# Kernel tuning notes

Measured on AMD Instinct MI355X. Metric: run time of the kernel, lower is better.

Reference implementation:

```python
import jax, jax.numpy as jnp
import numpy as np


def setup_inputs() -> dict:
    key = jax.random.key(0)
    k1, k2, k3, k4, k5 = jax.random.split(key, 5)
    B, C, V, D, O = 8, 64, 25000, 12, 64
    x = jax.random.normal(k1, (B, C, V), dtype=jnp.float32)
    nbr_idx = jax.random.randint(k2, (B, V, D), 0, V, dtype=jnp.int32)
    # true 1-ring valence in [1, D]
    deg = jax.random.randint(k3, (B, V), 1, D + 1, dtype=jnp.int32)
    # conv weight [O, C, 1, 2] flattened to [O, C, 2], fan-in init scale
    W = jax.random.normal(k4, (O, C, 2), dtype=jnp.float32) * (1.0 / np.sqrt(C * 2))
    b = jax.random.normal(k5, (O,), dtype=jnp.float32) * 0.01
    return {"x": x, "nbr_idx": nbr_idx, "deg": deg, "W": W, "b": b}


def reference(x, nbr_idx, deg, W, b):
    # x: [B, C, V]; nbr_idx: [B, V, D] padded 1-ring; deg: [B, V] valid count
    B, C, V = x.shape
    D = nbr_idx.shape[-1]
    # gather neighbor features: [B, C, V, D]
    gathered = jax.vmap(lambda xb, ib: xb[:, ib])(x, nbr_idx)
    mask = (jnp.arange(D, dtype=deg.dtype)[None, None, :] < deg[:, :, None])  # [B, V, D]
    maskf = mask.astype(x.dtype)[:, None, :, :]  # [B, 1, V, D]
    denom = jnp.maximum(deg, 1).astype(x.dtype)[:, None, :]  # [B, 1, V]
    nbr_mean = jnp.sum(gathered * maskf, axis=-1) / denom  # [B, C, V]
    # G: [B, C, V, 2] = (self feature, 1-ring mean); conv2d kernel (1,2)
    G = jnp.stack([x, nbr_mean], axis=-1)
    out = jnp.einsum('bcvk,ock->bov', G, W) + b[None, :, None]
    return out[..., None]  # [B, O, V, 1]
```

## Files before the change

kernel.cpp:

```cpp
#include <hip/hip_runtime.h>
#include <stdint.h>


#define NB 8
#define NC 64
#define NV 25000
#define ND 12
#define NO 64
#define VTILE 128
#define NGT 196
#define GVT 782

typedef uint32_t u32x4 __attribute__((ext_vector_type(4)));
typedef uint32_t u32x2 __attribute__((ext_vector_type(2)));
typedef __bf16  bf16x8 __attribute__((ext_vector_type(8)));
typedef float   f32x4  __attribute__((ext_vector_type(4)));

__device__ inline uint32_t bf16pack(float a, float b) {
    uint32_t ua = __float_as_uint(a), ub = __float_as_uint(b);
    ua = (ua + 0x7fffu + ((ua >> 16) & 1u)) >> 16;
    ub = (ub + 0x7fffu + ((ub >> 16) & 1u)) >> 16;
    return ua | (ub << 16);
}
__device__ inline float blo(uint32_t u) { return __uint_as_float(u << 16); }
__device__ inline float bhi(uint32_t u) { return __uint_as_float(u & 0xffff0000u); }

__global__ __launch_bounds__(256) void wt_kernel(const float* __restrict__ W,
                                                 uint32_t* __restrict__ Wcb) {
    int i = blockIdx.x * 256 + threadIdx.x;
    int m = i >> 5;
    int c = (i & 31) * 2;
    int k = m >> 6;
    int o = m & 63;
    float s0 = W[o * (NC * 2) + c * 2 + k];
    float s1 = W[o * (NC * 2) + (c + 1) * 2 + k];
    Wcb[i] = bf16pack(s0, s1);
}

__global__ __launch_bounds__(256) void ygemm_mfma(const float* __restrict__ x,
                                                  const uint32_t* __restrict__ Wcb,
                                                  const float* __restrict__ bias,
                                                  uint32_t* __restrict__ y0,
                                                  uint32_t* __restrict__ y1) {
    __shared__ uint32_t xt[VTILE * 36];

    const int b = blockIdx.x & 7;
    const int tile = blockIdx.x >> 3;
    const int vbase = tile * VTILE;
    const int tid = threadIdx.x;
    const float* xb = x + (size_t)b * NC * NV;

    {
        const int vl = tid & 127;
        const int ph = tid >> 7;
        int vg = vbase + vl;
        if (vg >= NV) vg = NV - 1;
#pragma unroll
        for (int r = 0; r < 16; ++r) {
            const int p = r * 2 + ph;
            const int c = p * 2;
            float s0 = __builtin_nontemporal_load(xb + (size_t)c * NV + vg);
            float s1 = __builtin_nontemporal_load(xb + (size_t)(c + 1) * NV + vg);
            xt[vl * 36 + p] = bf16pack(s0, s1);
        }
    }
    __syncthreads();

    const int lane = tid & 63, wave = tid >> 6;
    const int l15 = lane & 15, lq = lane >> 4;

    union BF { u32x4 q; bf16x8 v; } bf[2][2];
#pragma unroll
    for (int s = 0; s < 2; ++s) {
        const int vloc = (wave * 2 + s) * 16 + l15;
#pragma unroll
        for (int kt = 0; kt < 2; ++kt)
            bf[s][kt].q = *reinterpret_cast<const u32x4*>(&xt[vloc * 36 + kt * 16 + lq * 4]);
    }

    f32x4 acc[2][8];
#pragma unroll
    for (int s = 0; s < 2; ++s)
#pragma unroll
        for (int mt = 0; mt < 8; ++mt) acc[s][mt] = (f32x4){0.f, 0.f, 0.f, 0.f};

#pragma unroll
    for (int kt = 0; kt < 2; ++kt) {
#pragma unroll
        for (int mt = 0; mt < 8; ++mt) {
            union { u32x4 q; bf16x8 v; } au;
            au.q = *(const u32x4*)(Wcb + (size_t)(mt * 16 + l15) * 32 + kt * 16 + lq * 4);
#pragma unroll
            for (int s = 0; s < 2; ++s)
                acc[s][mt] = __builtin_amdgcn_mfma_f32_16x16x32_bf16(au.v, bf[s][kt].v,
                                                                     acc[s][mt], 0, 0, 0);
        }
    }

#pragma unroll
    for (int s = 0; s < 2; ++s) {
        const int v = vbase + (wave * 2 + s) * 16 + l15;
        if (v < NV) {
            uint32_t* yr0 = y0 + ((size_t)b * NV + v) * 32;
            uint32_t* yr1 = y1 + ((size_t)b * NV + v) * 32;
#pragma unroll
            for (int mt = 0; mt < 8; ++mt) {
                const int mo = mt * 16 + lq * 4;
                f32x4 a = acc[s][mt];
                if (mt < 4) {
                    const float* bp = bias + mo;
                    a[0] += bp[0]; a[1] += bp[1]; a[2] += bp[2]; a[3] += bp[3];
                    u32x2 p = {bf16pack(a[0], a[1]), bf16pack(a[2], a[3])};
                    __builtin_nontemporal_store(p, (u32x2*)(yr0 + (mo >> 1)));
                } else {
                    u32x2 p = {bf16pack(a[0], a[1]), bf16pack(a[2], a[3])};
                    *(u32x2*)(yr1 + ((mo - 64) >> 1)) = p;
                }
            }
        }
    }
}

__global__ __launch_bounds__(256) void gather_out(const int* __restrict__ nbr,
                                                  const int* __restrict__ deg,
                                                  const uint32_t* __restrict__ y0,
                                                  const uint32_t* __restrict__ y1,
                                                  float* __restrict__ out) {
    __shared__ float lds[32 * 68];

    const int b = blockIdx.x & 7;
    const int tile = blockIdx.x >> 3;
    const int lane = threadIdx.x & 63;
    const int wave = threadIdx.x >> 6;
    const int s = lane >> 3;
    const int j = lane & 7;
    const int vloc = wave * 8 + s;
    const int v = tile * 32 + vloc;
    const int vc = v < NV ? v : NV - 1;
    const size_t bv = (size_t)b * NV + vc;

    int idxr[ND];
    {
        const int4* p = reinterpret_cast<const int4*>(nbr + bv * ND);
        int4 a0 = p[0], a1 = p[1], a2 = p[2];
        idxr[0] = a0.x; idxr[1] = a0.y; idxr[2]  = a0.z; idxr[3]  = a0.w;
        idxr[4] = a1.x; idxr[5] = a1.y; idxr[6]  = a1.z; idxr[7]  = a1.w;
        idxr[8] = a2.x; idxr[9] = a2.y; idxr[10] = a2.z; idxr[11] = a2.w;
    }
    const int dg = deg[bv];
    const float inv = 1.0f / (float)dg;
    const uint32_t* y1b = y1 + (size_t)b * NV * 32;

    u32x4 su = __builtin_nontemporal_load(
        reinterpret_cast<const u32x4*>(y0 + bv * 32) + j);

    u32x4 rows[ND];
#pragma unroll
    for (int d = 0; d < ND; ++d) {
        if (d < dg)
            rows[d] = *(reinterpret_cast<const u32x4*>(y1b + (size_t)idxr[d] * 32) + j);
    }

    float ns[8];
#pragma unroll
    for (int t = 0; t < 8; ++t) ns[t] = 0.0f;
#pragma unroll
    for (int d = 0; d < ND; ++d) {
        if (d < dg) {
            u32x4 u = rows[d];
            ns[0] += blo(u[0]); ns[1] += bhi(u[0]);
            ns[2] += blo(u[1]); ns[3] += bhi(u[1]);
            ns[4] += blo(u[2]); ns[5] += bhi(u[2]);
            ns[6] += blo(u[3]); ns[7] += bhi(u[3]);
        }
    }

    {
        float f[8];
        f[0] = __builtin_fmaf(inv, ns[0], blo(su[0]));
        f[1] = __builtin_fmaf(inv, ns[1], bhi(su[0]));
        f[2] = __builtin_fmaf(inv, ns[2], blo(su[1]));
        f[3] = __builtin_fmaf(inv, ns[3], bhi(su[1]));
        f[4] = __builtin_fmaf(inv, ns[4], blo(su[2]));
        f[5] = __builtin_fmaf(inv, ns[5], bhi(su[2]));
        f[6] = __builtin_fmaf(inv, ns[6], blo(su[3]));
        f[7] = __builtin_fmaf(inv, ns[7], bhi(su[3]));
        f32x4 w0 = {f[0], f[1], f[2], f[3]};
        f32x4 w1 = {f[4], f[5], f[6], f[7]};
        *reinterpret_cast<f32x4*>(&lds[vloc * 68 + j * 8])     = w0;
        *reinterpret_cast<f32x4*>(&lds[vloc * 68 + j * 8 + 4]) = w1;
    }
    __syncthreads();

    {
        const int vl = threadIdx.x & 31;
        const int o8 = threadIdx.x >> 5;
        const int vv = tile * 32 + vl;
        if (vv < NV) {
            float* ob = out + (size_t)b * NO * NV + vv;
#pragma unroll
            for (int oo = 0; oo < 8; ++oo) {
                const int o = oo * 8 + o8;
                __builtin_nontemporal_store(lds[vl * 68 + o], ob + (size_t)o * NV);
            }
        }
    }
}

__global__ __launch_bounds__(64) void fallback_kernel(const float* __restrict__ x,
                                                      const int* __restrict__ nbr,
                                                      const int* __restrict__ deg,
                                                      const float* __restrict__ W,
                                                      const float* __restrict__ bias,
                                                      float* __restrict__ out) {
    const int bvi = blockIdx.x;
    const int b = bvi / NV, v = bvi % NV;
    const int o = threadIdx.x;
    const int degv = deg[bvi];
    const float inv = 1.0f / (float)degv;
    float acc = bias[o];
    for (int c = 0; c < NC; ++c) {
        const float* xc = x + ((size_t)b * NC + c) * NV;
        float m = 0.0f;
        for (int d = 0; d < degv; ++d) m += xc[nbr[(size_t)bvi * ND + d]];
        acc += W[o * (NC * 2) + c * 2] * xc[v] + W[o * (NC * 2) + c * 2 + 1] * (m * inv);
    }
    out[((size_t)b * NO + o) * NV + v] = acc;
}

extern "C" void kernel_launch(void* const* d_in, const int* in_sizes, int n_in,
                              void* d_out, int out_size, void* d_ws, size_t ws_size,
                              hipStream_t stream) {
    const float* x    = (const float*)d_in[0];
    const int*   nbr  = (const int*)d_in[1];
    const int*   deg  = (const int*)d_in[2];
    const float* W    = (const float*)d_in[3];
    const float* bias = (const float*)d_in[4];
    float* out = (float*)d_out;

    const size_t wcb_dw = 4096;
    const size_t yplane = (size_t)NB * NV * 32;
    const size_t need = (wcb_dw + 2 * yplane) * 4;
    if (ws_size >= need) {
        uint32_t* Wcb = (uint32_t*)d_ws;
        uint32_t* y0 = Wcb + wcb_dw;
        uint32_t* y1 = y0 + yplane;
        wt_kernel<<<dim3(16), 256, 0, stream>>>(W, Wcb);
        ygemm_mfma<<<dim3(NB * NGT), 256, 0, stream>>>(x, Wcb, bias, y0, y1);
        gather_out<<<dim3(NB * GVT), 256, 0, stream>>>(nbr, deg, y0, y1, out);
    } else {
        fallback_kernel<<<dim3(NB * NV), 64, 0, stream>>>(x, nbr, deg, W, bias, out);
    }
}
```

Before: 170.7 us.

## Move self-term GEMM into gather kernel, store transposed bf16 x instead of y0

The first kernel now computes only the neighbor projection y1 and also writes a transposed bf16 copy of x. The gather kernel computes the self projection W0·x plus bias with MFMA from that copy and stages it in LDS before adding the neighbor mean. The intermediate buffer is the same size as the old y0 plane, so bytes written and read do not change. The GEMM work is split across the two kernels, adding MFMA work and an extra barrier to the gather kernel, which may overlap its latency-bound neighbor loads.

```diff
diff --git a/kernel.cpp b/kernel.cpp
--- a/kernel.cpp
+++ b/kernel.cpp
@@ -7,8 +7,8 @@
 #define NV 25000
 #define ND 12
 #define NO 64
-#define VTILE 128
-#define NGT 196
+#define VROW 32
+#define ATL 391
 #define GVT 782
 
 typedef uint32_t u32x4 __attribute__((ext_vector_type(4)));
@@ -37,93 +37,80 @@
     Wcb[i] = bf16pack(s0, s1);
 }
 
-__global__ __launch_bounds__(256) void ygemm_mfma(const float* __restrict__ x,
+__global__ __launch_bounds__(256) void xty1(const float* __restrict__ x,
+                                            const uint32_t* __restrict__ Wcb,
+                                            uint32_t* __restrict__ xt,
+                                            uint32_t* __restrict__ y1) {
+    __shared__ uint32_t lb[64 * 36];
+    const int b = blockIdx.x & 7;
+    const int tile = blockIdx.x >> 3;
+    const int vbase = tile * 64;
+    const int lane = threadIdx.x & 63, wave = threadIdx.x >> 6;
+    const float* xb = x + (size_t)b * NC * NV;
+
+    {
+        int vg = vbase + lane;
+        if (vg >= NV) vg = NV - 1;
+#pragma unroll
+        for (int rr = 0; rr < 8; ++rr) {
+            const int c = wave * 16 + rr * 2;
+            float s0 = __builtin_nontemporal_load(xb + (size_t)c * NV + vg);
+            float s1 = __builtin_nontemporal_load(xb + (size_t)(c + 1) * NV + vg);
+            lb[lane * 36 + wave * 8 + rr] = bf16pack(s0, s1);
+        }
+    }
+    __syncthreads();
+
+    {
+        const int vl = threadIdx.x >> 2, q = threadIdx.x & 3;
+        const int vo = vbase + vl;
+        if (vo < NV) {
+            u32x4 w0 = *reinterpret_cast<const u32x4*>(&lb[vl * 36 + q * 8]);
+            u32x4 w1 = *reinterpret_cast<const u32x4*>(&lb[vl * 36 + q * 8 + 4]);
+            uint32_t* dst = xt + ((size_t)b * NV + vo) * VROW + q * 8;
+            *reinterpret_cast<u32x4*>(dst)     = w0;
+            *reinterpret_cast<u32x4*>(dst + 4) = w1;
+        }
+    }
+
+    const int l15 = lane & 15, lq = lane >> 4;
+    union BF { u32x4 q; bf16x8 v; } bf[2];
+#pragma unroll
+    for (int kt = 0; kt < 2; ++kt)
+        bf[kt].q = *reinterpret_cast<const u32x4*>(
+            &lb[(wave * 16 + l15) * 36 + kt * 16 + lq * 4]);
+
+    f32x4 acc[4];
+#pragma unroll
+    for (int mt = 0; mt < 4; ++mt) acc[mt] = (f32x4){0.f, 0.f, 0.f, 0.f};
+
+#pragma unroll
+    for (int kt = 0; kt < 2; ++kt) {
+#pragma unroll
+        for (int mt = 0; mt < 4; ++mt) {
+            union { u32x4 q; bf16x8 v; } au;
+            au.q = *(const u32x4*)(Wcb + (size_t)(64 + mt * 16 + l15) * 32 + kt * 16 + lq * 4);
+            acc[mt] = __builtin_amdgcn_mfma_f32_16x16x32_bf16(au.v, bf[kt].v, acc[mt], 0, 0, 0);
+        }
+    }
+
+    const int v = vbase + wave * 16 + l15;
+    if (v < NV) {
+        uint32_t* yr = y1 + ((size_t)b * NV + v) * VROW;
+#pragma unroll
+        for (int mt = 0; mt < 4; ++mt) {
+            f32x4 a = acc[mt];
+            u32x2 p = {bf16pack(a[0], a[1]), bf16pack(a[2], a[3])};
+            *(u32x2*)(yr + mt * 8 + lq * 2) = p;
+        }
+    }
+}
+
+__global__ __launch_bounds__(256) void gather_out(const int* __restrict__ nbr,
+                                                  const int* __restrict__ deg,
+                                                  const uint32_t* __restrict__ xt,
                                                   const uint32_t* __restrict__ Wcb,
                                                   const float* __restrict__ bias,
-                                                  uint32_t* __restrict__ y0,
-                                                  uint32_t* __restrict__ y1) {
-    __shared__ uint32_t xt[VTILE * 36];
-
-    const int b = blockIdx.x & 7;
-    const int tile = blockIdx.x >> 3;
-    const int vbase = tile * VTILE;
-    const int tid = threadIdx.x;
-    const float* xb = x + (size_t)b * NC * NV;
-
-    {
-        const int vl = tid & 127;
-        const int ph = tid >> 7;
-        int vg = vbase + vl;
-        if (vg >= NV) vg = NV - 1;
-#pragma unroll
-        for (int r = 0; r < 16; ++r) {
-            const int p = r * 2 + ph;
-            const int c = p * 2;
-            float s0 = __builtin_nontemporal_load(xb + (size_t)c * NV + vg);
-            float s1 = __builtin_nontemporal_load(xb + (size_t)(c + 1) * NV + vg);
-            xt[vl * 36 + p] = bf16pack(s0, s1);
-        }
-    }
-    __syncthreads();
-
-    const int lane = tid & 63, wave = tid >> 6;
-    const int l15 = lane & 15, lq = lane >> 4;
-
-    union BF { u32x4 q; bf16x8 v; } bf[2][2];
-#pragma unroll
-    for (int s = 0; s < 2; ++s) {
-        const int vloc = (wave * 2 + s) * 16 + l15;
-#pragma unroll
-        for (int kt = 0; kt < 2; ++kt)
-            bf[s][kt].q = *reinterpret_cast<const u32x4*>(&xt[vloc * 36 + kt * 16 + lq * 4]);
-    }
-
-    f32x4 acc[2][8];
-#pragma unroll
-    for (int s = 0; s < 2; ++s)
-#pragma unroll
-        for (int mt = 0; mt < 8; ++mt) acc[s][mt] = (f32x4){0.f, 0.f, 0.f, 0.f};
-
-#pragma unroll
-    for (int kt = 0; kt < 2; ++kt) {
-#pragma unroll
-        for (int mt = 0; mt < 8; ++mt) {
-            union { u32x4 q; bf16x8 v; } au;
-            au.q = *(const u32x4*)(Wcb + (size_t)(mt * 16 + l15) * 32 + kt * 16 + lq * 4);
-#pragma unroll
-            for (int s = 0; s < 2; ++s)
-                acc[s][mt] = __builtin_amdgcn_mfma_f32_16x16x32_bf16(au.v, bf[s][kt].v,
-                                                                     acc[s][mt], 0, 0, 0);
-        }
-    }
-
-#pragma unroll
-    for (int s = 0; s < 2; ++s) {
-        const int v = vbase + (wave * 2 + s) * 16 + l15;
-        if (v < NV) {
-            uint32_t* yr0 = y0 + ((size_t)b * NV + v) * 32;
-            uint32_t* yr1 = y1 + ((size_t)b * NV + v) * 32;
-#pragma unroll
-            for (int mt = 0; mt < 8; ++mt) {
-                const int mo = mt * 16 + lq * 4;
-                f32x4 a = acc[s][mt];
-                if (mt < 4) {
-                    const float* bp = bias + mo;
-                    a[0] += bp[0]; a[1] += bp[1]; a[2] += bp[2]; a[3] += bp[3];
-                    u32x2 p = {bf16pack(a[0], a[1]), bf16pack(a[2], a[3])};
-                    __builtin_nontemporal_store(p, (u32x2*)(yr0 + (mo >> 1)));
-                } else {
-                    u32x2 p = {bf16pack(a[0], a[1]), bf16pack(a[2], a[3])};
-                    *(u32x2*)(yr1 + ((mo - 64) >> 1)) = p;
-                }
-            }
-        }
-    }
-}
-
-__global__ __launch_bounds__(256) void gather_out(const int* __restrict__ nbr,
-                                                  const int* __restrict__ deg,
-                                                  const uint32_t* __restrict__ y0,
                                                   const uint32_t* __restrict__ y1,
                                                   float* __restrict__ out) {
     __shared__ float lds[32 * 68];
@@ -132,9 +119,9 @@
     const int tile = blockIdx.x >> 3;
     const int lane = threadIdx.x & 63;
     const int wave = threadIdx.x >> 6;
-    const int s = lane >> 3;
+    const int s8 = lane >> 3;
     const int j = lane & 7;
-    const int vloc = wave * 8 + s;
+    const int vloc = wave * 8 + s8;
     const int v = tile * 32 + vloc;
     const int vc = v < NV ? v : NV - 1;
     const size_t bv = (size_t)b * NV + vc;
@@ -149,17 +136,53 @@
     }
     const int dg = deg[bv];
     const float inv = 1.0f / (float)dg;
-    const uint32_t* y1b = y1 + (size_t)b * NV * 32;
-
-    u32x4 su = __builtin_nontemporal_load(
-        reinterpret_cast<const u32x4*>(y0 + bv * 32) + j);
+    const uint32_t* y1b = y1 + (size_t)b * NV * VROW;
+
+    const int l15 = lane & 15, lq = lane >> 4;
+    {
+        const uint32_t* xtb = xt + (size_t)b * NV * VROW;
+        union BF { u32x4 q; bf16x8 v; } bfr[2][2];
+#pragma unroll
+        for (int s = 0; s < 2; ++s) {
+            int vv = tile * 32 + s * 16 + l15;
+            if (vv >= NV) vv = NV - 1;
+            const uint32_t* xr = xtb + (size_t)vv * VROW;
+#pragma unroll
+            for (int kt = 0; kt < 2; ++kt)
+                bfr[s][kt].q = *reinterpret_cast<const u32x4*>(xr + kt * 16 + lq * 4);
+        }
+        f32x4 acc[2];
+        acc[0] = (f32x4){0.f, 0.f, 0.f, 0.f};
+        acc[1] = (f32x4){0.f, 0.f, 0.f, 0.f};
+#pragma unroll
+        for (int kt = 0; kt < 2; ++kt) {
+            union { u32x4 q; bf16x8 v; } au;
+            au.q = *(const u32x4*)(Wcb + (size_t)(wave * 16 + l15) * 32 + kt * 16 + lq * 4);
+#pragma unroll
+            for (int s = 0; s < 2; ++s)
+                acc[s] = __builtin_amdgcn_mfma_f32_16x16x32_bf16(au.v, bfr[s][kt].v,
+                                                                 acc[s], 0, 0, 0);
+        }
+        const f32x4 bq = *reinterpret_cast<const f32x4*>(bias + wave * 16 + lq * 4);
+#pragma unroll
+        for (int s = 0; s < 2; ++s) {
+            const int vr = s * 16 + l15;
+            const int ob = wave * 16 + lq * 4;
+            lds[vr * 68 + ob + 0] = acc[s][0] + bq[0];
+            lds[vr * 68 + ob + 1] = acc[s][1] + bq[1];
+            lds[vr * 68 + ob + 2] = acc[s][2] + bq[2];
+            lds[vr * 68 + ob + 3] = acc[s][3] + bq[3];
+        }
+    }
 
     u32x4 rows[ND];
 #pragma unroll
     for (int d = 0; d < ND; ++d) {
         if (d < dg)
-            rows[d] = *(reinterpret_cast<const u32x4*>(y1b + (size_t)idxr[d] * 32) + j);
-    }
+            rows[d] = *(reinterpret_cast<const u32x4*>(y1b + (size_t)idxr[d] * VROW) + j);
+    }
+
+    __syncthreads();
 
     float ns[8];
 #pragma unroll
@@ -176,19 +199,18 @@
     }
 
     {
-        float f[8];
-        f[0] = __builtin_fmaf(inv, ns[0], blo(su[0]));
-        f[1] = __builtin_fmaf(inv, ns[1], bhi(su[0]));
-        f[2] = __builtin_fmaf(inv, ns[2], blo(su[1]));
-        f[3] = __builtin_fmaf(inv, ns[3], bhi(su[1]));
-        f[4] = __builtin_fmaf(inv, ns[4], blo(su[2]));
-        f[5] = __builtin_fmaf(inv, ns[5], bhi(su[2]));
-        f[6] = __builtin_fmaf(inv, ns[6], blo(su[3]));
-        f[7] = __builtin_fmaf(inv, ns[7], bhi(su[3]));
-        f32x4 w0 = {f[0], f[1], f[2], f[3]};
-        f32x4 w1 = {f[4], f[5], f[6], f[7]};
-        *reinterpret_cast<f32x4*>(&lds[vloc * 68 + j * 8])     = w0;
-        *reinterpret_cast<f32x4*>(&lds[vloc * 68 + j * 8 + 4]) = w1;
+        f32x4 c0 = *reinterpret_cast<const f32x4*>(&lds[vloc * 68 + j * 8]);
+        f32x4 c1 = *reinterpret_cast<const f32x4*>(&lds[vloc * 68 + j * 8 + 4]);
+        c0[0] = __builtin_fmaf(inv, ns[0], c0[0]);
+        c0[1] = __builtin_fmaf(inv, ns[1], c0[1]);
+        c0[2] = __builtin_fmaf(inv, ns[2], c0[2]);
+        c0[3] = __builtin_fmaf(inv, ns[3], c0[3]);
+        c1[0] = __builtin_fmaf(inv, ns[4], c1[0]);
+        c1[1] = __builtin_fmaf(inv, ns[5], c1[1]);
+        c1[2] = __builtin_fmaf(inv, ns[6], c1[2]);
+        c1[3] = __builtin_fmaf(inv, ns[7], c1[3]);
+        *reinterpret_cast<f32x4*>(&lds[vloc * 68 + j * 8])     = c0;
+        *reinterpret_cast<f32x4*>(&lds[vloc * 68 + j * 8 + 4]) = c1;
     }
     __syncthreads();
 
@@ -239,15 +261,15 @@
     float* out = (float*)d_out;
 
     const size_t wcb_dw = 4096;
-    const size_t yplane = (size_t)NB * NV * 32;
-    const size_t need = (wcb_dw + 2 * yplane) * 4;
+    const size_t plane  = (size_t)NB * NV * VROW;
+    const size_t need = (wcb_dw + 2 * plane) * 4;
     if (ws_size >= need) {
         uint32_t* Wcb = (uint32_t*)d_ws;
-        uint32_t* y0 = Wcb + wcb_dw;
-        uint32_t* y1 = y0 + yplane;
+        uint32_t* xtb = Wcb + wcb_dw;
+        uint32_t* y1  = xtb + plane;
         wt_kernel<<<dim3(16), 256, 0, stream>>>(W, Wcb);
-        ygemm_mfma<<<dim3(NB * NGT), 256, 0, stream>>>(x, Wcb, bias, y0, y1);
-        gather_out<<<dim3(NB * GVT), 256, 0, stream>>>(nbr, deg, y0, y1, out);
+        xty1<<<dim3(NB * ATL), 256, 0, stream>>>(x, Wcb, xtb, y1);
+        gather_out<<<dim3(NB * GVT), 256, 0, stream>>>(nbr, deg, xtb, Wcb, bias, y1, out);
     } else {
         fallback_kernel<<<dim3(NB * NV), 64, 0, stream>>>(x, nbr, deg, W, bias, out);
     }
```

New measurement: 168.8 us. Within noise of the previous version (-1.1%).

## Shrink GEMM tiles and make gather persistent with prefetch and double-buffered LDS

Applied to the files above, without the earlier changes.

The projection GEMM now uses 64-vertex tiles with one 16-vertex MFMA slice per wave, and each thread stages its x values into LDS with vector writes. The gather kernel becomes a grid-stride persistent loop of 256 blocks per batch that prefetches the next tile's neighbour indices, degree and self row while the current neighbour rows are reduced. It alternates between two LDS buffers so only one barrier is needed per iteration. The goal is to hide index-load latency and cut launch and tail overhead, at the cost of more registers and fewer resident blocks.

```diff
diff --git a/kernel.cpp b/kernel.cpp
--- a/kernel.cpp
+++ b/kernel.cpp
@@ -7,9 +7,10 @@
 #define NV 25000
 #define ND 12
 #define NO 64
-#define VTILE 128
-#define NGT 196
-#define GVT 782
+#define VROW 32
+#define ATL 391
+#define NTB 782
+#define GTB 256
 
 typedef uint32_t u32x4 __attribute__((ext_vector_type(4)));
 typedef uint32_t u32x2 __attribute__((ext_vector_type(2)));
@@ -37,173 +38,194 @@
     Wcb[i] = bf16pack(s0, s1);
 }
 
-__global__ __launch_bounds__(256) void ygemm_mfma(const float* __restrict__ x,
-                                                  const uint32_t* __restrict__ Wcb,
-                                                  const float* __restrict__ bias,
-                                                  uint32_t* __restrict__ y0,
-                                                  uint32_t* __restrict__ y1) {
-    __shared__ uint32_t xt[VTILE * 36];
-
+__global__ __launch_bounds__(256) void ygemm3(const float* __restrict__ x,
+                                              const uint32_t* __restrict__ Wcb,
+                                              const float* __restrict__ bias,
+                                              uint32_t* __restrict__ y0,
+                                              uint32_t* __restrict__ y1) {
+    __shared__ uint32_t lb[64 * 36];
     const int b = blockIdx.x & 7;
     const int tile = blockIdx.x >> 3;
-    const int vbase = tile * VTILE;
-    const int tid = threadIdx.x;
+    const int vbase = tile * 64;
+    const int lane = threadIdx.x & 63, wave = threadIdx.x >> 6;
     const float* xb = x + (size_t)b * NC * NV;
 
     {
-        const int vl = tid & 127;
-        const int ph = tid >> 7;
-        int vg = vbase + vl;
+        int vg = vbase + lane;
         if (vg >= NV) vg = NV - 1;
-#pragma unroll
-        for (int r = 0; r < 16; ++r) {
-            const int p = r * 2 + ph;
-            const int c = p * 2;
+        uint32_t wb[8];
+#pragma unroll
+        for (int rr = 0; rr < 8; ++rr) {
+            const int c = wave * 16 + rr * 2;
             float s0 = __builtin_nontemporal_load(xb + (size_t)c * NV + vg);
             float s1 = __builtin_nontemporal_load(xb + (size_t)(c + 1) * NV + vg);
-            xt[vl * 36 + p] = bf16pack(s0, s1);
-        }
+            wb[rr] = bf16pack(s0, s1);
+        }
+        uint32_t* dst = &lb[lane * 36 + wave * 8];
+        *reinterpret_cast<u32x4*>(dst)     = (u32x4){wb[0], wb[1], wb[2], wb[3]};
+        *reinterpret_cast<u32x4*>(dst + 4) = (u32x4){wb[4], wb[5], wb[6], wb[7]};
     }
     __syncthreads();
 
-    const int lane = tid & 63, wave = tid >> 6;
     const int l15 = lane & 15, lq = lane >> 4;
-
-    union BF { u32x4 q; bf16x8 v; } bf[2][2];
-#pragma unroll
-    for (int s = 0; s < 2; ++s) {
-        const int vloc = (wave * 2 + s) * 16 + l15;
-#pragma unroll
-        for (int kt = 0; kt < 2; ++kt)
-            bf[s][kt].q = *reinterpret_cast<const u32x4*>(&xt[vloc * 36 + kt * 16 + lq * 4]);
-    }
-
-    f32x4 acc[2][8];
-#pragma unroll
-    for (int s = 0; s < 2; ++s)
-#pragma unroll
-        for (int mt = 0; mt < 8; ++mt) acc[s][mt] = (f32x4){0.f, 0.f, 0.f, 0.f};
+    union BF { u32x4 q; bf16x8 v; } bfr[2];
+#pragma unroll
+    for (int kt = 0; kt < 2; ++kt)
+        bfr[kt].q = *reinterpret_cast<const u32x4*>(
+            &lb[(wave * 16 + l15) * 36 + kt * 16 + lq * 4]);
+
+    f32x4 acc[2][4];
+#pragma unroll
+    for (int p = 0; p < 2; ++p)
+#pragma unroll
+        for (int mt = 0; mt < 4; ++mt) acc[p][mt] = (f32x4){0.f, 0.f, 0.f, 0.f};
 
 #pragma unroll
     for (int kt = 0; kt < 2; ++kt) {
 #pragma unroll
-        for (int mt = 0; mt < 8; ++mt) {
-            union { u32x4 q; bf16x8 v; } au;
-            au.q = *(const u32x4*)(Wcb + (size_t)(mt * 16 + l15) * 32 + kt * 16 + lq * 4);
-#pragma unroll
-            for (int s = 0; s < 2; ++s)
-                acc[s][mt] = __builtin_amdgcn_mfma_f32_16x16x32_bf16(au.v, bf[s][kt].v,
-                                                                     acc[s][mt], 0, 0, 0);
-        }
-    }
-
-#pragma unroll
-    for (int s = 0; s < 2; ++s) {
-        const int v = vbase + (wave * 2 + s) * 16 + l15;
-        if (v < NV) {
-            uint32_t* yr0 = y0 + ((size_t)b * NV + v) * 32;
-            uint32_t* yr1 = y1 + ((size_t)b * NV + v) * 32;
-#pragma unroll
-            for (int mt = 0; mt < 8; ++mt) {
-                const int mo = mt * 16 + lq * 4;
-                f32x4 a = acc[s][mt];
-                if (mt < 4) {
-                    const float* bp = bias + mo;
-                    a[0] += bp[0]; a[1] += bp[1]; a[2] += bp[2]; a[3] += bp[3];
-                    u32x2 p = {bf16pack(a[0], a[1]), bf16pack(a[2], a[3])};
-                    __builtin_nontemporal_store(p, (u32x2*)(yr0 + (mo >> 1)));
-                } else {
-                    u32x2 p = {bf16pack(a[0], a[1]), bf16pack(a[2], a[3])};
-                    *(u32x2*)(yr1 + ((mo - 64) >> 1)) = p;
+        for (int p = 0; p < 2; ++p) {
+#pragma unroll
+            for (int mt = 0; mt < 4; ++mt) {
+                union { u32x4 q; bf16x8 v; } au;
+                au.q = *(const u32x4*)(Wcb + (size_t)(p * 64 + mt * 16 + l15) * 32
+                                           + kt * 16 + lq * 4);
+                acc[p][mt] = __builtin_amdgcn_mfma_f32_16x16x32_bf16(au.v, bfr[kt].v,
+                                                                     acc[p][mt], 0, 0, 0);
+            }
+        }
+    }
+
+    const int v = vbase + wave * 16 + l15;
+    if (v < NV) {
+        uint32_t* yr0 = y0 + ((size_t)b * NV + v) * VROW;
+        uint32_t* yr1 = y1 + ((size_t)b * NV + v) * VROW;
+#pragma unroll
+        for (int mt = 0; mt < 4; ++mt) {
+            f32x4 a0 = acc[0][mt];
+            const float* bp = bias + mt * 16 + lq * 4;
+            a0[0] += bp[0]; a0[1] += bp[1]; a0[2] += bp[2]; a0[3] += bp[3];
+            u32x2 p0 = {bf16pack(a0[0], a0[1]), bf16pack(a0[2], a0[3])};
+            __builtin_nontemporal_store(p0, (u32x2*)(yr0 + mt * 8 + lq * 2));
+            f32x4 a1 = acc[1][mt];
+            u32x2 p1 = {bf16pack(a1[0], a1[1]), bf16pack(a1[2], a1[3])};
+            *(u32x2*)(yr1 + mt * 8 + lq * 2) = p1;
+        }
+    }
+}
+
+__global__ __launch_bounds__(256) void gather3(const int* __restrict__ nbr,
+                                               const int* __restrict__ deg,
+                                               const uint32_t* __restrict__ y0,
+                                               const uint32_t* __restrict__ y1,
+                                               float* __restrict__ out) {
+    __shared__ float lds[2][32 * 68];
+
+    const int b = blockIdx.x & 7;
+    const int t0 = blockIdx.x >> 3;
+    const int lane = threadIdx.x & 63;
+    const int wave = threadIdx.x >> 6;
+    const int s8 = lane >> 3;
+    const int j = lane & 7;
+    const int vloc = wave * 8 + s8;
+
+    const int* nbrb = nbr + (size_t)b * NV * ND;
+    const int* degb = deg + (size_t)b * NV;
+    const uint32_t* y0b = y0 + (size_t)b * NV * VROW;
+    const uint32_t* y1b = y1 + (size_t)b * NV * VROW;
+    float* outb = out + (size_t)b * NO * NV;
+
+    int idx[ND];
+    int dg;
+    u32x4 su;
+    {
+        int v = t0 * 32 + vloc;
+        const int vc = v < NV ? v : NV - 1;
+        const int4* p = reinterpret_cast<const int4*>(nbrb + (size_t)vc * ND);
+        int4 a0 = p[0], a1 = p[1], a2 = p[2];
+        idx[0] = a0.x; idx[1] = a0.y; idx[2]  = a0.z; idx[3]  = a0.w;
+        idx[4] = a1.x; idx[5] = a1.y; idx[6]  = a1.z; idx[7]  = a1.w;
+        idx[8] = a2.x; idx[9] = a2.y; idx[10] = a2.z; idx[11] = a2.w;
+        dg = degb[vc];
+        su = *(reinterpret_cast<const u32x4*>(y0b + (size_t)vc * VROW) + j);
+    }
+
+    int buf = 0;
+    for (int t = t0; t < NTB; t += GTB) {
+        u32x4 rows[ND];
+#pragma unroll
+        for (int d = 0; d < ND; ++d) {
+            if (d < dg)
+                rows[d] = *(reinterpret_cast<const u32x4*>(
+                                y1b + (size_t)idx[d] * VROW) + j);
+        }
+
+        const int tn = (t + GTB < NTB) ? t + GTB : t;
+        int idxn[ND];
+        int dgn;
+        u32x4 sun;
+        {
+            int v = tn * 32 + vloc;
+            const int vc = v < NV ? v : NV - 1;
+            const int4* p = reinterpret_cast<const int4*>(nbrb + (size_t)vc * ND);
+            int4 a0 = p[0], a1 = p[1], a2 = p[2];
+            idxn[0] = a0.x; idxn[1] = a0.y; idxn[2]  = a0.z; idxn[3]  = a0.w;
+            idxn[4] = a1.x; idxn[5] = a1.y; idxn[6]  = a1.z; idxn[7]  = a1.w;
+            idxn[8] = a2.x; idxn[9] = a2.y; idxn[10] = a2.z; idxn[11] = a2.w;
+            dgn = degb[vc];
+            sun = *(reinterpret_cast<const u32x4*>(y0b + (size_t)vc * VROW) + j);
+        }
+
+        const float inv = 1.0f / (float)dg;
+        float ns[8];
+#pragma unroll
+        for (int k = 0; k < 8; ++k) ns[k] = 0.0f;
+#pragma unroll
+        for (int d = 0; d < ND; ++d) {
+            if (d < dg) {
+                u32x4 u = rows[d];
+                ns[0] += blo(u[0]); ns[1] += bhi(u[0]);
+                ns[2] += blo(u[1]); ns[3] += bhi(u[1]);
+                ns[4] += blo(u[2]); ns[5] += bhi(u[2]);
+                ns[6] += blo(u[3]); ns[7] += bhi(u[3]);
+            }
+        }
+
+        {
+            float f[8];
+            f[0] = __builtin_fmaf(inv, ns[0], blo(su[0]));
+            f[1] = __builtin_fmaf(inv, ns[1], bhi(su[0]));
+            f[2] = __builtin_fmaf(inv, ns[2], blo(su[1]));
+            f[3] = __builtin_fmaf(inv, ns[3], bhi(su[1]));
+            f[4] = __builtin_fmaf(inv, ns[4], blo(su[2]));
+            f[5] = __builtin_fmaf(inv, ns[5], bhi(su[2]));
+            f[6] = __builtin_fmaf(inv, ns[6], blo(su[3]));
+            f[7] = __builtin_fmaf(inv, ns[7], bhi(su[3]));
+            f32x4 w0 = {f[0], f[1], f[2], f[3]};
+            f32x4 w1 = {f[4], f[5], f[6], f[7]};
+            *reinterpret_cast<f32x4*>(&lds[buf][vloc * 68 + j * 8])     = w0;
+            *reinterpret_cast<f32x4*>(&lds[buf][vloc * 68 + j * 8 + 4]) = w1;
+        }
+        __syncthreads();
+
+        {
+            const int vl = threadIdx.x & 31;
+            const int o8 = threadIdx.x >> 5;
+            const int vv = t * 32 + vl;
+            if (vv < NV) {
+#pragma unroll
+                for (int oo = 0; oo < 8; ++oo) {
+                    const int o = oo * 8 + o8;
+                    __builtin_nontemporal_store(lds[buf][vl * 68 + o],
+                                                outb + (size_t)o * NV + vv);
                 }
             }
         }
-    }
-}
-
-__global__ __launch_bounds__(256) void gather_out(const int* __restrict__ nbr,
-                                                  const int* __restrict__ deg,
-                                                  const uint32_t* __restrict__ y0,
-                                                  const uint32_t* __restrict__ y1,
-                                                  float* __restrict__ out) {
-    __shared__ float lds[32 * 68];
-
-    const int b = blockIdx.x & 7;
-    const int tile = blockIdx.x >> 3;
-    const int lane = threadIdx.x & 63;
-    const int wave = threadIdx.x >> 6;
-    const int s = lane >> 3;
-    const int j = lane & 7;
-    const int vloc = wave * 8 + s;
-    const int v = tile * 32 + vloc;
-    const int vc = v < NV ? v : NV - 1;
-    const size_t bv = (size_t)b * NV + vc;
-
-    int idxr[ND];
-    {
-        const int4* p = reinterpret_cast<const int4*>(nbr + bv * ND);
-        int4 a0 = p[0], a1 = p[1], a2 = p[2];
-        idxr[0] = a0.x; idxr[1] = a0.y; idxr[2]  = a0.z; idxr[3]  = a0.w;
-        idxr[4] = a1.x; idxr[5] = a1.y; idxr[6]  = a1.z; idxr[7]  = a1.w;
-        idxr[8] = a2.x; idxr[9] = a2.y; idxr[10] = a2.z; idxr[11] = a2.w;
-    }
-    const int dg = deg[bv];
-    const float inv = 1.0f / (float)dg;
-    const uint32_t* y1b = y1 + (size_t)b * NV * 32;
-
-    u32x4 su = __builtin_nontemporal_load(
-        reinterpret_cast<const u32x4*>(y0 + bv * 32) + j);
-
-    u32x4 rows[ND];
-#pragma unroll
-    for (int d = 0; d < ND; ++d) {
-        if (d < dg)
-            rows[d] = *(reinterpret_cast<const u32x4*>(y1b + (size_t)idxr[d] * 32) + j);
-    }
-
-    float ns[8];
-#pragma unroll
-    for (int t = 0; t < 8; ++t) ns[t] = 0.0f;
-#pragma unroll
-    for (int d = 0; d < ND; ++d) {
-        if (d < dg) {
-            u32x4 u = rows[d];
-            ns[0] += blo(u[0]); ns[1] += bhi(u[0]);
-            ns[2] += blo(u[1]); ns[3] += bhi(u[1]);
-            ns[4] += blo(u[2]); ns[5] += bhi(u[2]);
-            ns[6] += blo(u[3]); ns[7] += bhi(u[3]);
-        }
-    }
-
-    {
-        float f[8];
-        f[0] = __builtin_fmaf(inv, ns[0], blo(su[0]));
-        f[1] = __builtin_fmaf(inv, ns[1], bhi(su[0]));
-        f[2] = __builtin_fmaf(inv, ns[2], blo(su[1]));
-        f[3] = __builtin_fmaf(inv, ns[3], bhi(su[1]));
-        f[4] = __builtin_fmaf(inv, ns[4], blo(su[2]));
-        f[5] = __builtin_fmaf(inv, ns[5], bhi(su[2]));
-        f[6] = __builtin_fmaf(inv, ns[6], blo(su[3]));
-        f[7] = __builtin_fmaf(inv, ns[7], bhi(su[3]));
-        f32x4 w0 = {f[0], f[1], f[2], f[3]};
-        f32x4 w1 = {f[4], f[5], f[6], f[7]};
-        *reinterpret_cast<f32x4*>(&lds[vloc * 68 + j * 8])     = w0;
-        *reinterpret_cast<f32x4*>(&lds[vloc * 68 + j * 8 + 4]) = w1;
-    }
-    __syncthreads();
-
-    {
-        const int vl = threadIdx.x & 31;
-        const int o8 = threadIdx.x >> 5;
-        const int vv = tile * 32 + vl;
-        if (vv < NV) {
-            float* ob = out + (size_t)b * NO * NV + vv;
-#pragma unroll
-            for (int oo = 0; oo < 8; ++oo) {
-                const int o = oo * 8 + o8;
-                __builtin_nontemporal_store(lds[vl * 68 + o], ob + (size_t)o * NV);
-            }
-        }
+
+        buf ^= 1;
+        dg = dgn;
+        su = sun;
+#pragma unroll
+        for (int d = 0; d < ND; ++d) idx[d] = idxn[d];
     }
 }
 
@@ -239,15 +261,15 @@
     float* out = (float*)d_out;
 
     const size_t wcb_dw = 4096;
-    const size_t yplane = (size_t)NB * NV * 32;
-    const size_t need = (wcb_dw + 2 * yplane) * 4;
+    const size_t plane  = (size_t)NB * NV * VROW;
+    const size_t need = (wcb_dw + 2 * plane) * 4;
     if (ws_size >= need) {
         uint32_t* Wcb = (uint32_t*)d_ws;
-        uint32_t* y0 = Wcb + wcb_dw;
-        uint32_t* y1 = y0 + yplane;
+        uint32_t* y0  = Wcb + wcb_dw;
+        uint32_t* y1  = y0 + plane;
         wt_kernel<<<dim3(16), 256, 0, stream>>>(W, Wcb);
-        ygemm_mfma<<<dim3(NB * NGT), 256, 0, stream>>>(x, Wcb, bias, y0, y1);
-        gather_out<<<dim3(NB * GVT), 256, 0, stream>>>(nbr, deg, y0, y1, out);
+        ygemm3<<<dim3(NB * ATL), 256, 0, stream>>>(x, Wcb, bias, y0, y1);
+        gather3<<<dim3(NB * GTB), 256, 0, stream>>>(nbr, deg, y0, y1, out);
     } else {
         fallback_kernel<<<dim3(NB * NV), 64, 0, stream>>>(x, nbr, deg, W, bias, out);
     }
```

Result: slower. 188.2 us (+10.2%).
